# Optimization experiments

Measured on AMD Instinct MI355X. Metric: run time of the kernel, lower is better.

The kernel has to match this reference:

```python
import jax, jax.numpy as jnp
import numpy as np

B, T, D, H, S, PM = 2048, 128, 32, 256, 39, 12


def setup_inputs() -> dict:
    key = jax.random.key(0)
    ks = jax.random.split(key, 20)
    s = 0.05
    return {
        "x": jax.random.normal(ks[0], (B, T, D), jnp.float32),
        "latlons": jax.random.normal(ks[1], (B, 2), jnp.float32),
        "yearly_aggs": jax.random.normal(ks[2], (B, 37), jnp.float32),
        "pred_month": jax.random.uniform(ks[3], (B, PM), jnp.float32),
        # EA-LSTM cell parameters (Linear stores weight as [out,in])
        "Wf_i": jax.random.normal(ks[4], (H, D), jnp.float32) * s,
        "Wf_h": jax.random.normal(ks[5], (H, H), jnp.float32) * s,
        "bf_h": jnp.zeros((H,), jnp.float32),
        "Wu": jax.random.normal(ks[6], (H, S), jnp.float32) * s,
        "bu": jnp.zeros((H,), jnp.float32),
        "Wg_i": jax.random.normal(ks[7], (H, D), jnp.float32) * s,
        "Wg_h": jax.random.normal(ks[8], (H, H), jnp.float32) * s,
        "bg_h": jnp.zeros((H,), jnp.float32),
        "Wo_i": jax.random.normal(ks[9], (H, D), jnp.float32) * s,
        "Wo_h": jax.random.normal(ks[10], (H, H), jnp.float32) * s,
        "bo_h": jnp.zeros((H,), jnp.float32),
        # dense head: [268 -> 256 -> 1], no nonlinearity between layers (as in source)
        "Wd0": jax.random.normal(ks[11], (256, H + PM), jnp.float32) * s,
        "bd0": jnp.zeros((256,), jnp.float32),
        "Wd1": jax.random.normal(ks[12], (1, 256), jnp.float32) * s,
        "bd1": jnp.zeros((1,), jnp.float32),
    }


def reference(x, latlons, yearly_aggs, pred_month,
              Wf_i, Wf_h, bf_h, Wu, bu,
              Wg_i, Wg_h, bg_h, Wo_i, Wo_h, bo_h,
              Wd0, bd0, Wd1, bd1):
    x_s = jnp.concatenate([latlons, yearly_aggs], axis=-1)  # [B,S]
    i_gate = jax.nn.sigmoid(x_s @ Wu.T + bu)  # [B,H], static input gate

    # Precompute the input-to-gate projections for all timesteps (one big GEMM each)
    pf = jnp.einsum('btd,hd->tbh', x, Wf_i)  # [T,B,H]
    pg = jnp.einsum('btd,hd->tbh', x, Wg_i)
    po = jnp.einsum('btd,hd->tbh', x, Wo_i)

    h0 = jnp.zeros((x.shape[0], Wf_h.shape[0]), x.dtype)
    c0 = jnp.zeros_like(h0)

    def step(carry, inp):
        h, c = carry
        pf_t, pg_t, po_t = inp
        f = jax.nn.sigmoid(pf_t + h @ Wf_h.T + bf_h)
        g = jnp.tanh(pg_t + h @ Wg_h.T + bg_h)
        o = jax.nn.sigmoid(po_t + h @ Wo_h.T + bo_h)
        c1 = f * c + i_gate * g
        h1 = o * jnp.tanh(c1)
        return (h1, c1), None

    (h_last, _), _ = jax.lax.scan(step, (h0, c0), (pf, pg, po))

    # only the last hidden state feeds the dense head (dropout p=0 -> identity)
    z = jnp.concatenate([h_last, pred_month], axis=-1)  # [B, H+12]
    z = z @ Wd0.T + bd0
    z = z @ Wd1.T + bd1
    return z  # [B,1]
```

## Files before the change

kernel.cpp:

```cpp
#include <hip/hip_runtime.h>

typedef __bf16 bf16x8 __attribute__((ext_vector_type(8)));
typedef float  f32x4  __attribute__((ext_vector_type(4)));
typedef int    v4i    __attribute__((ext_vector_type(4)));

#define LOG2E 1.4426950408889634f

__device__ __forceinline__ float fexp(float x){ return __builtin_amdgcn_exp2f(x * LOG2E); }
__device__ __forceinline__ float sigm(float x){ return __builtin_amdgcn_rcpf(1.0f + fexp(-x)); }
__device__ __forceinline__ float ftanh(float x){
  float r = __builtin_amdgcn_rcpf(1.0f + __builtin_amdgcn_exp2f(-2.0f*LOG2E*x));
  return 2.0f*r - 1.0f;
}
__device__ __forceinline__ f32x4 MFMA(bf16x8 a, bf16x8 b, f32x4 c){
  return __builtin_amdgcn_mfma_f32_16x16x32_bf16(a, b, c, 0, 0, 0);
}
#define BC(w) __builtin_bit_cast(v4i, (w))

#define GRP_A(LEAD, A_, KT_) asm volatile(LEAD                  \
    "v_mfma_f32_16x16x32_bf16 %0, %6, %7, %0\n\t"               \
    "v_mfma_f32_16x16x32_bf16 %1, %6, %8, %1\n\t"               \
    "v_mfma_f32_16x16x32_bf16 %2, %6, %9, %2\n\t"               \
    "v_mfma_f32_16x16x32_bf16 %3, %6, %10, %3\n\t"              \
    "v_mfma_f32_16x16x32_bf16 %4, %6, %11, %4\n\t"              \
    "v_mfma_f32_16x16x32_bf16 %5, %6, %12, %5\n\t"              \
    "s_nop 3"                                                   \
    : "+v"(acc0),"+v"(acc1),"+v"(acc2),"+v"(acc3),"+v"(acc4),"+v"(acc5) \
    : "v"(A_), "a"(awf[(KT_)]),"a"(awf[(KT_)+5]),"a"(awf[(KT_)+10]),    \
      "a"(awf[(KT_)+15]),"a"(awf[(KT_)+20]),"a"(awf[(KT_)+25]))

#define GRP_V(A_, O_) asm volatile(                             \
    "v_mfma_f32_16x16x32_bf16 %0, %6, %7, %0\n\t"               \
    "v_mfma_f32_16x16x32_bf16 %1, %6, %8, %1\n\t"               \
    "v_mfma_f32_16x16x32_bf16 %2, %6, %9, %2\n\t"               \
    "v_mfma_f32_16x16x32_bf16 %3, %6, %10, %3\n\t"              \
    "v_mfma_f32_16x16x32_bf16 %4, %6, %11, %4\n\t"              \
    "v_mfma_f32_16x16x32_bf16 %5, %6, %12, %5\n\t"              \
    "s_nop 3"                                                   \
    : "+v"(acc0),"+v"(acc1),"+v"(acc2),"+v"(acc3),"+v"(acc4),"+v"(acc5) \
    : "v"(A_), "v"(wvf[(O_)]),"v"(wvf[(O_)+2]),"v"(wvf[(O_)+4]),        \
      "v"(wvf[(O_)+6]),"v"(wvf[(O_)+8]),"v"(wvf[(O_)+10]))

#define GRP_LX(A7_, AX_) asm volatile(                          \
    "ds_read_b128 %6, %14\n\t"                                  \
    "ds_read_b128 %7, %14 offset:1024\n\t"                      \
    "ds_read_b128 %8, %14 offset:16384\n\t"                     \
    "ds_read_b128 %9, %14 offset:17408\n\t"                     \
    "ds_read_b128 %10, %14 offset:32768\n\t"                    \
    "ds_read_b128 %11, %14 offset:33792\n\t"                    \
    "s_waitcnt lgkmcnt(0)\n\t"                                  \
    "v_mfma_f32_16x16x32_bf16 %0, %12, %6, %0\n\t"              \
    "v_mfma_f32_16x16x32_bf16 %1, %12, %7, %1\n\t"              \
    "v_mfma_f32_16x16x32_bf16 %2, %12, %8, %2\n\t"              \
    "v_mfma_f32_16x16x32_bf16 %3, %12, %9, %3\n\t"              \
    "v_mfma_f32_16x16x32_bf16 %4, %12, %10, %4\n\t"             \
    "v_mfma_f32_16x16x32_bf16 %5, %12, %11, %5\n\t"             \
    "ds_read_b128 %6, %15\n\t"                                  \
    "ds_read_b128 %7, %15 offset:1024\n\t"                      \
    "ds_read_b128 %8, %15 offset:16384\n\t"                     \
    "ds_read_b128 %9, %15 offset:17408\n\t"                     \
    "ds_read_b128 %10, %15 offset:32768\n\t"                    \
    "ds_read_b128 %11, %15 offset:33792\n\t"                    \
    "s_waitcnt lgkmcnt(0)\n\t"                                  \
    "v_mfma_f32_16x16x32_bf16 %0, %13, %6, %0\n\t"              \
    "v_mfma_f32_16x16x32_bf16 %1, %13, %7, %1\n\t"              \
    "v_mfma_f32_16x16x32_bf16 %2, %13, %8, %2\n\t"              \
    "v_mfma_f32_16x16x32_bf16 %3, %13, %9, %3\n\t"              \
    "v_mfma_f32_16x16x32_bf16 %4, %13, %10, %4\n\t"             \
    "v_mfma_f32_16x16x32_bf16 %5, %13, %11, %5\n\t"             \
    "s_nop 3"                                                   \
    : "+v"(acc0),"+v"(acc1),"+v"(acc2),"+v"(acc3),"+v"(acc4),"+v"(acc5), \
      "=&v"(t0),"=&v"(t1),"=&v"(t2),"=&v"(t3),"=&v"(t4),"=&v"(t5)        \
    : "v"(A7_), "v"(AX_), "v"(waddr0), "v"(waddr1))

#define BARRIER() asm volatile("s_waitcnt lgkmcnt(0)\n\ts_barrier" ::: "memory")

__global__ void
__attribute__((amdgpu_flat_work_group_size(512,512), amdgpu_waves_per_eu(2,2)))
ealstm_kernel(
    const float* __restrict__ x,      const float* __restrict__ latlons,
    const float* __restrict__ yearly, const float* __restrict__ pm,
    const float* __restrict__ Wf_i, const float* __restrict__ Wf_h, const float* __restrict__ bf_h,
    const float* __restrict__ Wu,   const float* __restrict__ bu,
    const float* __restrict__ Wg_i, const float* __restrict__ Wg_h, const float* __restrict__ bg_h,
    const float* __restrict__ Wo_i, const float* __restrict__ Wo_h, const float* __restrict__ bo_h,
    const float* __restrict__ Wd0,  const float* __restrict__ bd0,
    const float* __restrict__ Wd1,  const float* __restrict__ bd1,
    float* __restrict__ out)
{
  __shared__ __align__(16) __bf16 hbuf[2][4096];
  __shared__ __align__(16) __bf16 xbuf[2][16*40];
  __shared__ __align__(16) __bf16 wlds[2*48*512];
  __shared__ __align__(16) float  xs[16*64];

  const int tid  = threadIdx.x;
  const int w    = tid >> 6;
  const int lane = tid & 63;
  const int q    = lane >> 4;
  const int l    = lane & 15;
  const int wgb  = blockIdx.x * 8;

  const float* Wh[3] = {Wf_h, Wg_h, Wo_h};
  const float* Wi[3] = {Wf_i, Wg_i, Wo_i};

  for(int idx = tid; idx < 16*64; idx += 512){
    int m = idx >> 6, k = idx & 63;
    float v = 0.0f;
    if(m < 8){
      int b = wgb + m;
      if(k < 2) v = latlons[b*2 + k];
      else if(k < 39) v = yearly[b*37 + (k-2)];
    }
    xs[idx] = v;
  }
  for(int idx = tid; idx < 2*4096; idx += 512) ((__bf16*)hbuf)[idx] = (__bf16)0.0f;
  {
    int buf = tid >> 8, r = 8 + ((tid >> 5) & 7), c = tid & 31;
    xbuf[buf][r*40 + c] = (__bf16)0.0f;
  }
  if(tid < 256){
    int m = tid >> 5, k = tid & 31;
    xbuf[0][m*40 + k] = (__bf16)x[(size_t)(wgb + m)*4096 + k];
  }
  for(int grp = tid; grp < 2*48*64; grp += 512){
    int frag = grp >> 6, ln = grp & 63;
    int kk = frag / 48, f2 = frag % 48;
    int g = f2 >> 4, nt = f2 & 15;
    int q2 = ln >> 4, l2 = ln & 15;
    int cc = nt*16 + l2;
    const float* p = (kk == 0) ? (Wh[g] + cc*256 + 224 + q2*8)
                               : (Wi[g] + cc*32  + q2*8);
    bf16x8 v;
    #pragma unroll
    for(int j=0;j<8;j++) v[j] = (__bf16)p[j];
    *(bf16x8*)&wlds[frag*512 + ln*8] = v;
  }

  const int  srcl = lane & 31;
  const bool lo   = lane < 32;
  const int  qq4  = (q & 1) * 4;
  const int  colw = w*32 + ((lane & 32) >> 1) + l;
  const int  hwb  = (colw >> 5)*512 + qq4*32 + ((colw >> 3) & 3)*8 + (colw & 7);
  const unsigned waddr0 = (unsigned)(unsigned long long)&wlds[(0*48 + w*2)*512 + lane*8];
  const unsigned waddr1 = waddr0 + 49152u;
  const float b3f = bf_h[colw], b3g = bg_h[colw], b3o = bo_h[colw];

  __syncthreads();

  f32x4 igv;
  {
    float bu0 = bu[w*32 + l], bu1 = bu[w*32 + 16 + l];
    f32x4 iga0 = {bu0,bu0,bu0,bu0};
    f32x4 iga1 = {bu1,bu1,bu1,bu1};
    #pragma unroll
    for(int kt=0; kt<2; kt++){
      bf16x8 a;
      const float* xr = &xs[l*64 + kt*32 + q*8];
      #pragma unroll
      for(int j=0;j<8;j++) a[j] = (__bf16)xr[j];
      #pragma unroll
      for(int n=0;n<2;n++){
        int cc = w*32 + n*16 + l;
        bf16x8 b;
        #pragma unroll
        for(int j=0;j<8;j++){
          int k = kt*32 + q*8 + j;
          b[j] = (__bf16)((k < 39) ? Wu[cc*39 + k] : 0.0f);
        }
        if(n == 0) iga0 = MFMA(a, b, iga0); else iga1 = MFMA(a, b, iga1);
      }
    }
    #pragma unroll
    for(int i=0;i<4;i++){
      float s0 = sigm(iga0[i]);
      float s1 = __shfl(sigm(iga1[i]), srcl);
      igv[i] = lo ? s0 : s1;
    }
  }

  v4i wvf[12];
  #pragma unroll
  for(int f = 0; f < 12; f++){
    int gn = f >> 1, kt = 5 + (f & 1);
    int g = gn >> 1, n = gn & 1;
    int cc = w*32 + n*16 + l;
    const float* p = Wh[g] + cc*256 + kt*32 + q*8;
    f32x4 v0 = *(const f32x4*)p;
    f32x4 v1 = *(const f32x4*)(p + 4);
    bf16x8 v;
    v[0]=(__bf16)v0[0]; v[1]=(__bf16)v0[1]; v[2]=(__bf16)v0[2]; v[3]=(__bf16)v0[3];
    v[4]=(__bf16)v1[0]; v[5]=(__bf16)v1[1]; v[6]=(__bf16)v1[2]; v[7]=(__bf16)v1[3];
    wvf[f] = BC(v);
    if((f & 3) == 3) asm volatile("" ::: "memory");
  }
  v4i awf[30];
  #pragma unroll
  for(int f = 0; f < 30; f++){
    int gn = f / 5, kt = f % 5;
    int g = gn >> 1, n = gn & 1;
    int cc = w*32 + n*16 + l;
    const float* p = Wh[g] + cc*256 + kt*32 + q*8;
    f32x4 v0 = *(const f32x4*)p;
    f32x4 v1 = *(const f32x4*)(p + 4);
    bf16x8 v;
    v[0]=(__bf16)v0[0]; v[1]=(__bf16)v0[1]; v[2]=(__bf16)v0[2]; v[3]=(__bf16)v0[3];
    v[4]=(__bf16)v1[0]; v[5]=(__bf16)v1[1]; v[6]=(__bf16)v1[2]; v[7]=(__bf16)v1[3];
    asm("" : "=a"(awf[f]) : "0"(BC(v)));
    if((f % 5) == 4) asm volatile("" ::: "memory");
  }

  f32x4 cst = {0.f, 0.f, 0.f, 0.f};

  const int xri = (lane >> 2)*40 + (lane & 3)*8;
  const float* xbase = x + (size_t)(wgb + (lane >> 2))*4096 + (lane & 3)*8;
  f32x4 pv0 = {0.f,0.f,0.f,0.f}, pv1 = {0.f,0.f,0.f,0.f};
  if(w == 7 && lane < 32){
    pv0 = *(const f32x4*)(xbase + 32);
    pv1 = *(const f32x4*)(xbase + 36);
  }
  asm volatile("" ::: "memory");

#define LSTM_STEP(T_, CUR_)                                                     \
  {                                                                             \
      \
      \
    if(w == 7 && lane < 32){                                                    \
      if((T_) < 127){                                                           \
        bf16x8 v;                                                               \
        v[0]=(__bf16)pv0[0]; v[1]=(__bf16)pv0[1]; v[2]=(__bf16)pv0[2]; v[3]=(__bf16)pv0[3]; \
        v[4]=(__bf16)pv1[0]; v[5]=(__bf16)pv1[1]; v[6]=(__bf16)pv1[2]; v[7]=(__bf16)pv1[3]; \
        *(bf16x8*)&xbuf[(CUR_) ^ 1][xri] = v;                                   \
      }                                                                         \
      if((T_) < 126){                                                           \
        pv0 = *(const f32x4*)(xbase + ((T_)+2)*32);                             \
        pv1 = *(const f32x4*)(xbase + ((T_)+2)*32 + 4);                         \
      }                                                                         \
    }                                                                           \
    asm volatile("" ::: "memory");                                              \
    f32x4 z4 = {0.f,0.f,0.f,0.f};                                               \
    v4i acc0 = BC(z4), acc1 = BC(z4), acc2 = BC(z4);                            \
    v4i acc3 = BC(z4), acc4 = BC(z4), acc5 = BC(z4);                            \
    v4i t0, t1, t2, t3, t4, t5;                                                 \
    const __bf16* hb = hbuf[CUR_];                                              \
    { v4i a = BC(*(const bf16x8*)&hb[0*512 + l*32 + q*8]); GRP_A("s_nop 3\n\t", a, 0); } \
    { v4i a = BC(*(const bf16x8*)&hb[1*512 + l*32 + q*8]); GRP_A("", a, 1); }   \
    { v4i a = BC(*(const bf16x8*)&hb[2*512 + l*32 + q*8]); GRP_A("", a, 2); }   \
    { v4i a = BC(*(const bf16x8*)&hb[3*512 + l*32 + q*8]); GRP_A("", a, 3); }   \
    { v4i a = BC(*(const bf16x8*)&hb[4*512 + l*32 + q*8]); GRP_A("", a, 4); }   \
    { v4i a = BC(*(const bf16x8*)&hb[5*512 + l*32 + q*8]); GRP_V(a, 0); }       \
    { v4i a = BC(*(const bf16x8*)&hb[6*512 + l*32 + q*8]); GRP_V(a, 1); }       \
    { v4i a7 = BC(*(const bf16x8*)&hb[7*512 + l*32 + q*8]);                     \
      v4i ax = BC(*(const bf16x8*)&xbuf[CUR_][l*40 + q*8]);                     \
      GRP_LX(a7, ax); }                                                         \
    asm volatile("s_nop 7\n\ts_nop 7\n\ts_nop 7"                                \
      : "+v"(acc0),"+v"(acc1),"+v"(acc2),"+v"(acc3),"+v"(acc4),"+v"(acc5));     \
    f32x4 a0 = __builtin_bit_cast(f32x4, acc0);                                 \
    f32x4 a1 = __builtin_bit_cast(f32x4, acc1);                                 \
    f32x4 a2 = __builtin_bit_cast(f32x4, acc2);                                 \
    f32x4 a3 = __builtin_bit_cast(f32x4, acc3);                                 \
    f32x4 a4 = __builtin_bit_cast(f32x4, acc4);                                 \
    f32x4 a5 = __builtin_bit_cast(f32x4, acc5);                                 \
    _Pragma("unroll")                                                           \
    for(int i=0;i<4;i++){                                                       \
      float f1 = __shfl(a1[i], srcl);                                           \
      float g1 = __shfl(a3[i], srcl);                                           \
      float o1 = __shfl(a5[i], srcl);                                           \
      float fv = sigm ((lo ? a0[i] : f1) + b3f);                                \
      float gv = ftanh((lo ? a2[i] : g1) + b3g);                                \
      float ov = sigm ((lo ? a4[i] : o1) + b3o);                                \
      float cc = fv * cst[i] + igv[i] * gv;                                     \
      cst[i] = cc;                                                              \
      hbuf[(CUR_) ^ 1][hwb + i*32] = (__bf16)(ov * ftanh(cc));                  \
    }                                                                           \
    BARRIER();                                                                  \
  }

  #pragma unroll 1
  for(int tt = 0; tt < 64; tt++){
    LSTM_STEP(2*tt,     0)
    LSTM_STEP(2*tt + 1, 1)
  }
#undef LSTM_STEP

  f32x4 hd[2];
  { f32x4 z4 = {0.f,0.f,0.f,0.f}; hd[0] = z4; hd[1] = z4; }
  #pragma unroll 2
  for(int kt=0; kt<8; kt++){
    bf16x8 a = *(const bf16x8*)&hbuf[0][kt*512 + l*32 + q*8];
    #pragma unroll
    for(int n=0;n<2;n++){
      int cc = w*32 + n*16 + l;
      const float* p = Wd0 + cc*268 + kt*32 + q*8;
      bf16x8 b;
      #pragma unroll
      for(int j=0;j<8;j++) b[j] = (__bf16)p[j];
      hd[n] = MFMA(a, b, hd[n]);
    }
  }
  {
    bf16x8 a;
    #pragma unroll
    for(int j=0;j<8;j++){
      int k2 = q*8 + j;
      a[j] = (__bf16)((l < 8 && k2 < 12) ? pm[(size_t)(wgb + l)*12 + k2] : 0.0f);
    }
    #pragma unroll
    for(int n=0;n<2;n++){
      int cc = w*32 + n*16 + l;
      bf16x8 b;
      #pragma unroll
      for(int j=0;j<8;j++){
        int k2 = q*8 + j;
        b[j] = (__bf16)((k2 < 12) ? Wd0[cc*268 + 256 + k2] : 0.0f);
      }
      hd[n] = MFMA(a, b, hd[n]);
    }
  }
  float* z1 = (float*)wlds;
  #pragma unroll
  for(int n=0;n<2;n++){
    int cc = w*32 + n*16 + l;
    float bb = bd0[cc];
    #pragma unroll
    for(int i=0;i<4;i++) z1[(q*4 + i)*264 + cc] = hd[n][i] + bb;
  }
  __syncthreads();
  if(tid < 256){
    int row = tid >> 5, seg = tid & 31;
    const float* zr = &z1[row*264 + seg*8];
    const float* wr = Wd1 + seg*8;
    float s = 0.0f;
    #pragma unroll
    for(int j=0;j<8;j++) s += zr[j] * wr[j];
    s += __shfl_xor(s, 1);
    s += __shfl_xor(s, 2);
    s += __shfl_xor(s, 4);
    s += __shfl_xor(s, 8);
    s += __shfl_xor(s, 16);
    if(seg == 0) out[wgb + row] = s + bd1[0];
  }
}

extern "C" void kernel_launch(void* const* d_in, const int* in_sizes, int n_in,
                              void* d_out, int out_size, void* d_ws, size_t ws_size,
                              hipStream_t stream) {
  const float* x       = (const float*)d_in[0];
  const float* latlons = (const float*)d_in[1];
  const float* yearly  = (const float*)d_in[2];
  const float* pm      = (const float*)d_in[3];
  const float* Wf_i    = (const float*)d_in[4];
  const float* Wf_h    = (const float*)d_in[5];
  const float* bf_h    = (const float*)d_in[6];
  const float* Wu      = (const float*)d_in[7];
  const float* bu      = (const float*)d_in[8];
  const float* Wg_i    = (const float*)d_in[9];
  const float* Wg_h    = (const float*)d_in[10];
  const float* bg_h    = (const float*)d_in[11];
  const float* Wo_i    = (const float*)d_in[12];
  const float* Wo_h    = (const float*)d_in[13];
  const float* bo_h    = (const float*)d_in[14];
  const float* Wd0     = (const float*)d_in[15];
  const float* bd0     = (const float*)d_in[16];
  const float* Wd1     = (const float*)d_in[17];
  const float* bd1     = (const float*)d_in[18];

  ealstm_kernel<<<dim3(256), dim3(512), 0, stream>>>(
      x, latlons, yearly, pm,
      Wf_i, Wf_h, bf_h, Wu, bu,
      Wg_i, Wg_h, bg_h, Wo_i, Wo_h, bo_h,
      Wd0, bd0, Wd1, bd1,
      (float*)d_out);
}
```

Baseline: 354.9 us.

## Software-pipeline LSTM step tail: overlap gate activations with remaining MFMAs and LDS reads

Restructures the recurrent step tail so the forget, cell and output gate accumulators are finished in separate stages. Each stage's nonlinearity (exp/rcp) and cross-half permlane32 swap runs while the next gate's MFMAs and the next LDS weight prefetches are in flight. Weight fragments for the first K tile are prefetched across the barrier into the next step. Two weight fragments move to AGPRs, and the x staging is split across two waves with 4-wide writes. The aim is to hide activation latency and LDS wait behind matrix work on the serial critical path. The cost is heavy hand-written asm with manual hazard nops and tighter register pressure.

```diff
diff --git a/kernel.cpp b/kernel.cpp
--- a/kernel.cpp
+++ b/kernel.cpp
@@ -1,6 +1,7 @@
 #include <hip/hip_runtime.h>
 
 typedef __bf16 bf16x8 __attribute__((ext_vector_type(8)));
+typedef __bf16 bf16x4 __attribute__((ext_vector_type(4)));
 typedef float  f32x4  __attribute__((ext_vector_type(4)));
 typedef int    v4i    __attribute__((ext_vector_type(4)));
 
@@ -41,37 +42,17 @@
     : "v"(A_), "v"(wvf[(O_)]),"v"(wvf[(O_)+2]),"v"(wvf[(O_)+4]),        \
       "v"(wvf[(O_)+6]),"v"(wvf[(O_)+8]),"v"(wvf[(O_)+10]))
 
-#define GRP_LX(A7_, AX_) asm volatile(                          \
-    "ds_read_b128 %6, %14\n\t"                                  \
-    "ds_read_b128 %7, %14 offset:1024\n\t"                      \
-    "ds_read_b128 %8, %14 offset:16384\n\t"                     \
-    "ds_read_b128 %9, %14 offset:17408\n\t"                     \
-    "ds_read_b128 %10, %14 offset:32768\n\t"                    \
-    "ds_read_b128 %11, %14 offset:33792\n\t"                    \
-    "s_waitcnt lgkmcnt(0)\n\t"                                  \
-    "v_mfma_f32_16x16x32_bf16 %0, %12, %6, %0\n\t"              \
-    "v_mfma_f32_16x16x32_bf16 %1, %12, %7, %1\n\t"              \
-    "v_mfma_f32_16x16x32_bf16 %2, %12, %8, %2\n\t"              \
-    "v_mfma_f32_16x16x32_bf16 %3, %12, %9, %3\n\t"              \
-    "v_mfma_f32_16x16x32_bf16 %4, %12, %10, %4\n\t"             \
-    "v_mfma_f32_16x16x32_bf16 %5, %12, %11, %5\n\t"             \
-    "ds_read_b128 %6, %15\n\t"                                  \
-    "ds_read_b128 %7, %15 offset:1024\n\t"                      \
-    "ds_read_b128 %8, %15 offset:16384\n\t"                     \
-    "ds_read_b128 %9, %15 offset:17408\n\t"                     \
-    "ds_read_b128 %10, %15 offset:32768\n\t"                    \
-    "ds_read_b128 %11, %15 offset:33792\n\t"                    \
-    "s_waitcnt lgkmcnt(0)\n\t"                                  \
-    "v_mfma_f32_16x16x32_bf16 %0, %13, %6, %0\n\t"              \
-    "v_mfma_f32_16x16x32_bf16 %1, %13, %7, %1\n\t"              \
-    "v_mfma_f32_16x16x32_bf16 %2, %13, %8, %2\n\t"              \
-    "v_mfma_f32_16x16x32_bf16 %3, %13, %9, %3\n\t"              \
-    "v_mfma_f32_16x16x32_bf16 %4, %13, %10, %4\n\t"             \
-    "v_mfma_f32_16x16x32_bf16 %5, %13, %11, %5\n\t"             \
+#define GRP_V6(A_) asm volatile(                                \
+    "v_mfma_f32_16x16x32_bf16 %0, %6, %7, %0\n\t"               \
+    "v_mfma_f32_16x16x32_bf16 %1, %6, %8, %1\n\t"               \
+    "v_mfma_f32_16x16x32_bf16 %2, %6, %9, %2\n\t"               \
+    "v_mfma_f32_16x16x32_bf16 %3, %6, %10, %3\n\t"              \
+    "v_mfma_f32_16x16x32_bf16 %4, %6, %11, %4\n\t"              \
+    "v_mfma_f32_16x16x32_bf16 %5, %6, %12, %5\n\t"              \
     "s_nop 3"                                                   \
-    : "+v"(acc0),"+v"(acc1),"+v"(acc2),"+v"(acc3),"+v"(acc4),"+v"(acc5), \
-      "=&v"(t0),"=&v"(t1),"=&v"(t2),"=&v"(t3),"=&v"(t4),"=&v"(t5)        \
-    : "v"(A7_), "v"(AX_), "v"(waddr0), "v"(waddr1))
+    : "+v"(acc0),"+v"(acc1),"+v"(acc2),"+v"(acc3),"+v"(acc4),"+v"(acc5) \
+    : "v"(A_), "v"(wvf[1]),"v"(wvf[3]),"v"(wvf[5]),"v"(wvf[7]),         \
+      "a"(aw6o0),"a"(aw6o1))
 
 #define BARRIER() asm volatile("s_waitcnt lgkmcnt(0)\n\ts_barrier" ::: "memory")
 
@@ -143,6 +124,8 @@
   const int  hwb  = (colw >> 5)*512 + qq4*32 + ((colw >> 3) & 3)*8 + (colw & 7);
   const unsigned waddr0 = (unsigned)(unsigned long long)&wlds[(0*48 + w*2)*512 + lane*8];
   const unsigned waddr1 = waddr0 + 49152u;
+  const unsigned hA0 = (unsigned)(unsigned long long)&hbuf[0][l*32 + q*8];
+  const unsigned xA0 = (unsigned)(unsigned long long)&xbuf[0][l*40 + q*8];
   const float b3f = bf_h[colw], b3g = bg_h[colw], b3o = bo_h[colw];
 
   __syncthreads();
@@ -179,6 +162,7 @@
   }
 
   v4i wvf[12];
+  v4i aw6o0, aw6o1;
   #pragma unroll
   for(int f = 0; f < 12; f++){
     int gn = f >> 1, kt = 5 + (f & 1);
@@ -190,7 +174,9 @@
     bf16x8 v;
     v[0]=(__bf16)v0[0]; v[1]=(__bf16)v0[1]; v[2]=(__bf16)v0[2]; v[3]=(__bf16)v0[3];
     v[4]=(__bf16)v1[0]; v[5]=(__bf16)v1[1]; v[6]=(__bf16)v1[2]; v[7]=(__bf16)v1[3];
-    wvf[f] = BC(v);
+    if(f == 9)       asm("" : "=a"(aw6o0) : "0"(BC(v)));
+    else if(f == 11) asm("" : "=a"(aw6o1) : "0"(BC(v)));
+    else             wvf[f] = BC(v);
     if((f & 3) == 3) asm volatile("" ::: "memory");
   }
   v4i awf[30];
@@ -211,36 +197,47 @@
 
   f32x4 cst = {0.f, 0.f, 0.f, 0.f};
 
-  const int xri = (lane >> 2)*40 + (lane & 3)*8;
-  const float* xbase = x + (size_t)(wgb + (lane >> 2))*4096 + (lane & 3)*8;
-  f32x4 pv0 = {0.f,0.f,0.f,0.f}, pv1 = {0.f,0.f,0.f,0.f};
-  if(w == 7 && lane < 32){
-    pv0 = *(const f32x4*)(xbase + 32);
-    pv1 = *(const f32x4*)(xbase + 36);
-  }
+  const int wio = (w == 7) ? 4 : 0;
+  const int xri = (lane >> 2)*40 + (lane & 3)*8 + wio;
+  const float* xbase = x + (size_t)(wgb + (lane >> 2))*4096 + (lane & 3)*8 + wio;
+  f32x4 pv = {0.f,0.f,0.f,0.f};
+  if(w >= 6 && lane < 32) pv = *(const f32x4*)(xbase + 32);
   asm volatile("" ::: "memory");
+
+  v4i t0, t1, t2, t3, t4, t5;
+  asm volatile(
+    "ds_read_b128 %0, %6\n\t"
+    "ds_read_b128 %1, %6 offset:1024\n\t"
+    "ds_read_b128 %2, %7\n\t"
+    "ds_read_b128 %3, %7 offset:1024\n\t"
+    "ds_read_b128 %4, %6 offset:16384\n\t"
+    "ds_read_b128 %5, %6 offset:17408"
+    : "=v"(t0),"=v"(t1),"=v"(t2),"=v"(t3),"=v"(t4),"=v"(t5)
+    : "v"(waddr0),"v"(waddr1));
 
 #define LSTM_STEP(T_, CUR_)                                                     \
   {                                                                             \
-      \
-      \
-    if(w == 7 && lane < 32){                                                    \
+    if(w >= 6 && lane < 32){                                                    \
       if((T_) < 127){                                                           \
-        bf16x8 v;                                                               \
-        v[0]=(__bf16)pv0[0]; v[1]=(__bf16)pv0[1]; v[2]=(__bf16)pv0[2]; v[3]=(__bf16)pv0[3]; \
-        v[4]=(__bf16)pv1[0]; v[5]=(__bf16)pv1[1]; v[6]=(__bf16)pv1[2]; v[7]=(__bf16)pv1[3]; \
-        *(bf16x8*)&xbuf[(CUR_) ^ 1][xri] = v;                                   \
+        bf16x4 v4;                                                              \
+        v4[0]=(__bf16)pv[0]; v4[1]=(__bf16)pv[1];                               \
+        v4[2]=(__bf16)pv[2]; v4[3]=(__bf16)pv[3];                               \
+        *(bf16x4*)&xbuf[(CUR_) ^ 1][xri] = v4;                                  \
       }                                                                         \
-      if((T_) < 126){                                                           \
-        pv0 = *(const f32x4*)(xbase + ((T_)+2)*32);                             \
-        pv1 = *(const f32x4*)(xbase + ((T_)+2)*32 + 4);                         \
-      }                                                                         \
+      if((T_) < 126) pv = *(const f32x4*)(xbase + ((T_)+2)*32);                 \
     }                                                                           \
     asm volatile("" ::: "memory");                                              \
+    v4i A7, Axv;                                                                \
+    {                                                                           \
+      unsigned hAc = hA0 + (CUR_)*8192u;                                        \
+      unsigned xAc = xA0 + (CUR_)*1280u;                                        \
+      asm volatile("ds_read_b128 %0, %2 offset:7168\n\t"                        \
+                   "ds_read_b128 %1, %3"                                        \
+                   : "=v"(A7), "=v"(Axv) : "v"(hAc), "v"(xAc));                 \
+    }                                                                           \
     f32x4 z4 = {0.f,0.f,0.f,0.f};                                               \
     v4i acc0 = BC(z4), acc1 = BC(z4), acc2 = BC(z4);                            \
     v4i acc3 = BC(z4), acc4 = BC(z4), acc5 = BC(z4);                            \
-    v4i t0, t1, t2, t3, t4, t5;                                                 \
     const __bf16* hb = hbuf[CUR_];                                              \
     { v4i a = BC(*(const bf16x8*)&hb[0*512 + l*32 + q*8]); GRP_A("s_nop 3\n\t", a, 0); } \
     { v4i a = BC(*(const bf16x8*)&hb[1*512 + l*32 + q*8]); GRP_A("", a, 1); }   \
@@ -248,30 +245,148 @@
     { v4i a = BC(*(const bf16x8*)&hb[3*512 + l*32 + q*8]); GRP_A("", a, 3); }   \
     { v4i a = BC(*(const bf16x8*)&hb[4*512 + l*32 + q*8]); GRP_A("", a, 4); }   \
     { v4i a = BC(*(const bf16x8*)&hb[5*512 + l*32 + q*8]); GRP_V(a, 0); }       \
-    { v4i a = BC(*(const bf16x8*)&hb[6*512 + l*32 + q*8]); GRP_V(a, 1); }       \
-    { v4i a7 = BC(*(const bf16x8*)&hb[7*512 + l*32 + q*8]);                     \
-      v4i ax = BC(*(const bf16x8*)&xbuf[CUR_][l*40 + q*8]);                     \
-      GRP_LX(a7, ax); }                                                         \
-    asm volatile("s_nop 7\n\ts_nop 7\n\ts_nop 7"                                \
-      : "+v"(acc0),"+v"(acc1),"+v"(acc2),"+v"(acc3),"+v"(acc4),"+v"(acc5));     \
-    f32x4 a0 = __builtin_bit_cast(f32x4, acc0);                                 \
-    f32x4 a1 = __builtin_bit_cast(f32x4, acc1);                                 \
-    f32x4 a2 = __builtin_bit_cast(f32x4, acc2);                                 \
-    f32x4 a3 = __builtin_bit_cast(f32x4, acc3);                                 \
-    f32x4 a4 = __builtin_bit_cast(f32x4, acc4);                                 \
-    f32x4 a5 = __builtin_bit_cast(f32x4, acc5);                                 \
-    _Pragma("unroll")                                                           \
-    for(int i=0;i<4;i++){                                                       \
-      float f1 = __shfl(a1[i], srcl);                                           \
-      float g1 = __shfl(a3[i], srcl);                                           \
-      float o1 = __shfl(a5[i], srcl);                                           \
-      float fv = sigm ((lo ? a0[i] : f1) + b3f);                                \
-      float gv = ftanh((lo ? a2[i] : g1) + b3g);                                \
-      float ov = sigm ((lo ? a4[i] : o1) + b3o);                                \
-      float cc = fv * cst[i] + igv[i] * gv;                                     \
-      cst[i] = cc;                                                              \
-      hbuf[(CUR_) ^ 1][hwb + i*32] = (__bf16)(ov * ftanh(cc));                  \
-    }                                                                           \
+    { v4i a = BC(*(const bf16x8*)&hb[6*512 + l*32 + q*8]); GRP_V6(a); }         \
+      \
+      \
+      \
+    asm volatile(                                                               \
+      "s_waitcnt lgkmcnt(0)\n\t"                                                \
+      "v_mfma_f32_16x16x32_bf16 %0, %6, %2, %0\n\t"                             \
+      "v_mfma_f32_16x16x32_bf16 %1, %6, %3, %1\n\t"                             \
+      "s_nop 2\n\t"                                                             \
+      "v_mfma_f32_16x16x32_bf16 %0, %7, %4, %0\n\t"                             \
+      "v_mfma_f32_16x16x32_bf16 %1, %7, %5, %1\n\t"                             \
+      "ds_read_b128 %2, %9 offset:16384\n\t"                                    \
+      "ds_read_b128 %3, %9 offset:17408\n\t"                                    \
+      "ds_read_b128 %4, %8 offset:32768\n\t"                                    \
+      "ds_read_b128 %5, %8 offset:33792\n\t"                                    \
+      "s_nop 7\n\t"                                                             \
+      "s_nop 7\n\t"                                                             \
+      "s_nop 7\n\t"                                                             \
+      "s_nop 7"                                                                 \
+      : "+v"(acc0),"+v"(acc1),"+v"(t0),"+v"(t1),"+v"(t2),"+v"(t3)               \
+      : "v"(A7),"v"(Axv),"v"(waddr0),"v"(waddr1));                              \
+    f32x4 vf0 = __builtin_bit_cast(f32x4, acc0);                                \
+    f32x4 vf1 = __builtin_bit_cast(f32x4, acc1);                                \
+    float fa0=vf0[0], fa1=vf0[1], fa2=vf0[2], fa3=vf0[3];                       \
+    float fb0=vf1[0], fb1=vf1[1], fb2=vf1[2], fb3=vf1[3];                       \
+     \
+    asm volatile(                                                               \
+      "v_mfma_f32_16x16x32_bf16 %0, %14, %10, %0\n\t"                           \
+      "v_mfma_f32_16x16x32_bf16 %1, %14, %11, %1\n\t"                           \
+      "s_nop 2\n\t"                                                             \
+      "v_permlane32_swap_b32 %2, %6\n\t"                                        \
+      "v_permlane32_swap_b32 %3, %7\n\t"                                        \
+      "v_permlane32_swap_b32 %4, %8\n\t"                                        \
+      "v_permlane32_swap_b32 %5, %9\n\t"                                        \
+      "v_add_f32 %2, %2, %16\n\t"                                               \
+      "v_add_f32 %3, %3, %16\n\t"                                               \
+      "v_add_f32 %4, %4, %16\n\t"                                               \
+      "v_add_f32 %5, %5, %16\n\t"                                               \
+      "v_mul_f32 %2, 0xbfb8aa3b, %2\n\t"                                        \
+      "v_mul_f32 %3, 0xbfb8aa3b, %3\n\t"                                        \
+      "v_mul_f32 %4, 0xbfb8aa3b, %4\n\t"                                        \
+      "v_mul_f32 %5, 0xbfb8aa3b, %5\n\t"                                        \
+      "v_exp_f32 %2, %2\n\t"                                                    \
+      "v_exp_f32 %3, %3\n\t"                                                    \
+      "v_exp_f32 %4, %4\n\t"                                                    \
+      "v_exp_f32 %5, %5\n\t"                                                    \
+      "v_add_f32 %2, 1.0, %2\n\t"                                               \
+      "v_add_f32 %3, 1.0, %3\n\t"                                               \
+      "v_add_f32 %4, 1.0, %4\n\t"                                               \
+      "v_add_f32 %5, 1.0, %5\n\t"                                               \
+      "v_rcp_f32 %2, %2\n\t"                                                    \
+      "v_rcp_f32 %3, %3\n\t"                                                    \
+      "v_rcp_f32 %4, %4\n\t"                                                    \
+      "v_rcp_f32 %5, %5\n\t"                                                    \
+      "s_waitcnt lgkmcnt(2)\n\t"                                                \
+      "v_mfma_f32_16x16x32_bf16 %0, %15, %12, %0\n\t"                           \
+      "v_mfma_f32_16x16x32_bf16 %1, %15, %13, %1\n\t"                           \
+      "ds_read_b128 %10, %17 offset:32768\n\t"                                  \
+      "ds_read_b128 %11, %17 offset:33792\n\t"                                  \
+      "s_nop 7\n\t"                                                             \
+      "s_nop 7\n\t"                                                             \
+      "s_nop 7\n\t"                                                             \
+      "s_nop 7"                                                                 \
+      : "+v"(acc2),"+v"(acc3),"+v"(fa0),"+v"(fa1),"+v"(fa2),"+v"(fa3),          \
+        "+v"(fb0),"+v"(fb1),"+v"(fb2),"+v"(fb3),"+v"(t4),"+v"(t5)               \
+      : "v"(t0),"v"(t1),"v"(A7),"v"(Axv),"v"(b3f),"v"(waddr1));                 \
+    f32x4 vg0 = __builtin_bit_cast(f32x4, acc2);                                \
+    f32x4 vg1 = __builtin_bit_cast(f32x4, acc3);                                \
+    float ga0=vg0[0], ga1=vg0[1], ga2=vg0[2], ga3=vg0[3];                       \
+    float gb0=vg1[0], gb1=vg1[1], gb2=vg1[2], gb3=vg1[3];                       \
+     \
+    asm volatile(                                                               \
+      "s_waitcnt lgkmcnt(2)\n\t"                                                \
+      "v_mfma_f32_16x16x32_bf16 %0, %16, %12, %0\n\t"                           \
+      "v_mfma_f32_16x16x32_bf16 %1, %16, %13, %1\n\t"                           \
+      "s_nop 2\n\t"                                                             \
+      "v_permlane32_swap_b32 %2, %6\n\t"                                        \
+      "v_permlane32_swap_b32 %3, %7\n\t"                                        \
+      "v_permlane32_swap_b32 %4, %8\n\t"                                        \
+      "v_permlane32_swap_b32 %5, %9\n\t"                                        \
+      "v_add_f32 %2, %2, %18\n\t"                                               \
+      "v_add_f32 %3, %3, %18\n\t"                                               \
+      "v_add_f32 %4, %4, %18\n\t"                                               \
+      "v_add_f32 %5, %5, %18\n\t"                                               \
+      "v_mul_f32 %2, 0xc038aa3b, %2\n\t"                                        \
+      "v_mul_f32 %3, 0xc038aa3b, %3\n\t"                                        \
+      "v_mul_f32 %4, 0xc038aa3b, %4\n\t"                                        \
+      "v_mul_f32 %5, 0xc038aa3b, %5\n\t"                                        \
+      "v_exp_f32 %2, %2\n\t"                                                    \
+      "v_exp_f32 %3, %3\n\t"                                                    \
+      "v_exp_f32 %4, %4\n\t"                                                    \
+      "v_exp_f32 %5, %5\n\t"                                                    \
+      "v_add_f32 %2, 1.0, %2\n\t"                                               \
+      "v_add_f32 %3, 1.0, %3\n\t"                                               \
+      "v_add_f32 %4, 1.0, %4\n\t"                                               \
+      "v_add_f32 %5, 1.0, %5\n\t"                                               \
+      "v_rcp_f32 %2, %2\n\t"                                                    \
+      "v_rcp_f32 %3, %3\n\t"                                                    \
+      "v_rcp_f32 %4, %4\n\t"                                                    \
+      "v_rcp_f32 %5, %5\n\t"                                                    \
+      "v_fma_f32 %2, %2, 2.0, -1.0\n\t"                                         \
+      "v_fma_f32 %3, %3, 2.0, -1.0\n\t"                                         \
+      "v_fma_f32 %4, %4, 2.0, -1.0\n\t"                                         \
+      "v_fma_f32 %5, %5, 2.0, -1.0\n\t"                                         \
+      "s_waitcnt lgkmcnt(0)\n\t"                                                \
+      "v_mfma_f32_16x16x32_bf16 %0, %17, %14, %0\n\t"                           \
+      "v_mfma_f32_16x16x32_bf16 %1, %17, %15, %1\n\t"                           \
+      "ds_read_b128 %10, %19\n\t"                                               \
+      "ds_read_b128 %11, %19 offset:1024\n\t"                                   \
+      "ds_read_b128 %12, %20\n\t"                                               \
+      "ds_read_b128 %13, %20 offset:1024\n\t"                                   \
+      "ds_read_b128 %14, %19 offset:16384\n\t"                                  \
+      "ds_read_b128 %15, %19 offset:17408\n\t"                                  \
+      "s_nop 7\n\t"                                                             \
+      "s_nop 7\n\t"                                                             \
+      "s_nop 7\n\t"                                                             \
+      "s_nop 7"                                                                 \
+      : "+v"(acc4),"+v"(acc5),"+v"(ga0),"+v"(ga1),"+v"(ga2),"+v"(ga3),          \
+        "+v"(gb0),"+v"(gb1),"+v"(gb2),"+v"(gb3),                                \
+        "+v"(t0),"+v"(t1),"+v"(t2),"+v"(t3),"+v"(t4),"+v"(t5)                   \
+      : "v"(A7),"v"(Axv),"v"(b3g),"v"(waddr0),"v"(waddr1));                     \
+    f32x4 vo0 = __builtin_bit_cast(f32x4, acc4);                                \
+    f32x4 vo1 = __builtin_bit_cast(f32x4, acc5);                                \
+    float oa0=vo0[0], oa1=vo0[1], oa2=vo0[2], oa3=vo0[3];                       \
+    float ob0=vo1[0], ob1=vo1[1], ob2=vo1[2], ob3=vo1[3];                       \
+    asm volatile(                                                               \
+      "s_nop 1\n\t"                                                             \
+      "v_permlane32_swap_b32 %0, %4\n\t"                                        \
+      "v_permlane32_swap_b32 %1, %5\n\t"                                        \
+      "v_permlane32_swap_b32 %2, %6\n\t"                                        \
+      "v_permlane32_swap_b32 %3, %7"                                            \
+      : "+v"(oa0),"+v"(oa1),"+v"(oa2),"+v"(oa3),                                \
+        "+v"(ob0),"+v"(ob1),"+v"(ob2),"+v"(ob3));                               \
+    __bf16* hbw = &hbuf[(CUR_) ^ 1][hwb];                                       \
+    { float ov = sigm(oa0 + b3o); float cc = fa0*cst[0] + igv[0]*ga0;           \
+      cst[0] = cc; hbw[0]  = (__bf16)(ov * ftanh(cc)); }                        \
+    { float ov = sigm(oa1 + b3o); float cc = fa1*cst[1] + igv[1]*ga1;           \
+      cst[1] = cc; hbw[32] = (__bf16)(ov * ftanh(cc)); }                        \
+    { float ov = sigm(oa2 + b3o); float cc = fa2*cst[2] + igv[2]*ga2;           \
+      cst[2] = cc; hbw[64] = (__bf16)(ov * ftanh(cc)); }                        \
+    { float ov = sigm(oa3 + b3o); float cc = fa3*cst[3] + igv[3]*ga3;           \
+      cst[3] = cc; hbw[96] = (__bf16)(ov * ftanh(cc)); }                        \
     BARRIER();                                                                  \
   }
 
```

Result: slower. 398.5 us (+12.3%).

## Split recurrent columns across 16 waves with all weights held in AGPRs

Applied to the files above, without the earlier changes.

Doubles the workgroup to 1024 threads (16 waves), so each wave owns 16 hidden columns instead of 32. That lets all recurrent and input weights for a wave sit in accumulation registers, which removes the LDS weight staging, the per-step LDS weight reads and the cross-lane shuffles that stitched two column tiles together. Each step now issues fewer MFMAs per wave, with more waves per CU contending at the barrier. The extra registers and the larger barrier group may cost occupancy or add sync overhead.

```diff
diff --git a/kernel.cpp b/kernel.cpp
--- a/kernel.cpp
+++ b/kernel.cpp
@@ -17,66 +17,26 @@
 }
 #define BC(w) __builtin_bit_cast(v4i, (w))
 
-#define GRP_A(LEAD, A_, KT_) asm volatile(LEAD                  \
-    "v_mfma_f32_16x16x32_bf16 %0, %6, %7, %0\n\t"               \
-    "v_mfma_f32_16x16x32_bf16 %1, %6, %8, %1\n\t"               \
-    "v_mfma_f32_16x16x32_bf16 %2, %6, %9, %2\n\t"               \
-    "v_mfma_f32_16x16x32_bf16 %3, %6, %10, %3\n\t"              \
-    "v_mfma_f32_16x16x32_bf16 %4, %6, %11, %4\n\t"              \
-    "v_mfma_f32_16x16x32_bf16 %5, %6, %12, %5\n\t"              \
+#define GRP3(LEAD, A_, KT_) asm volatile(LEAD                   \
+    "v_mfma_f32_16x16x32_bf16 %0, %3, %4, %0\n\t"               \
+    "v_mfma_f32_16x16x32_bf16 %1, %3, %5, %1\n\t"               \
+    "v_mfma_f32_16x16x32_bf16 %2, %3, %6, %2\n\t"               \
     "s_nop 3"                                                   \
-    : "+v"(acc0),"+v"(acc1),"+v"(acc2),"+v"(acc3),"+v"(acc4),"+v"(acc5) \
-    : "v"(A_), "a"(awf[(KT_)]),"a"(awf[(KT_)+5]),"a"(awf[(KT_)+10]),    \
-      "a"(awf[(KT_)+15]),"a"(awf[(KT_)+20]),"a"(awf[(KT_)+25]))
-
-#define GRP_V(A_, O_) asm volatile(                             \
-    "v_mfma_f32_16x16x32_bf16 %0, %6, %7, %0\n\t"               \
-    "v_mfma_f32_16x16x32_bf16 %1, %6, %8, %1\n\t"               \
-    "v_mfma_f32_16x16x32_bf16 %2, %6, %9, %2\n\t"               \
-    "v_mfma_f32_16x16x32_bf16 %3, %6, %10, %3\n\t"              \
-    "v_mfma_f32_16x16x32_bf16 %4, %6, %11, %4\n\t"              \
-    "v_mfma_f32_16x16x32_bf16 %5, %6, %12, %5\n\t"              \
+    : "+v"(accf),"+v"(accg),"+v"(acco)                          \
+    : "v"(A_), "a"(awh[(KT_)]), "a"(awh[(KT_)+8]), "a"(awh[(KT_)+16]))
+
+#define GRPX(A_) asm volatile(                                  \
+    "v_mfma_f32_16x16x32_bf16 %0, %3, %4, %0\n\t"               \
+    "v_mfma_f32_16x16x32_bf16 %1, %3, %5, %1\n\t"               \
+    "v_mfma_f32_16x16x32_bf16 %2, %3, %6, %2\n\t"               \
     "s_nop 3"                                                   \
-    : "+v"(acc0),"+v"(acc1),"+v"(acc2),"+v"(acc3),"+v"(acc4),"+v"(acc5) \
-    : "v"(A_), "v"(wvf[(O_)]),"v"(wvf[(O_)+2]),"v"(wvf[(O_)+4]),        \
-      "v"(wvf[(O_)+6]),"v"(wvf[(O_)+8]),"v"(wvf[(O_)+10]))
-
-#define GRP_LX(A7_, AX_) asm volatile(                          \
-    "ds_read_b128 %6, %14\n\t"                                  \
-    "ds_read_b128 %7, %14 offset:1024\n\t"                      \
-    "ds_read_b128 %8, %14 offset:16384\n\t"                     \
-    "ds_read_b128 %9, %14 offset:17408\n\t"                     \
-    "ds_read_b128 %10, %14 offset:32768\n\t"                    \
-    "ds_read_b128 %11, %14 offset:33792\n\t"                    \
-    "s_waitcnt lgkmcnt(0)\n\t"                                  \
-    "v_mfma_f32_16x16x32_bf16 %0, %12, %6, %0\n\t"              \
-    "v_mfma_f32_16x16x32_bf16 %1, %12, %7, %1\n\t"              \
-    "v_mfma_f32_16x16x32_bf16 %2, %12, %8, %2\n\t"              \
-    "v_mfma_f32_16x16x32_bf16 %3, %12, %9, %3\n\t"              \
-    "v_mfma_f32_16x16x32_bf16 %4, %12, %10, %4\n\t"             \
-    "v_mfma_f32_16x16x32_bf16 %5, %12, %11, %5\n\t"             \
-    "ds_read_b128 %6, %15\n\t"                                  \
-    "ds_read_b128 %7, %15 offset:1024\n\t"                      \
-    "ds_read_b128 %8, %15 offset:16384\n\t"                     \
-    "ds_read_b128 %9, %15 offset:17408\n\t"                     \
-    "ds_read_b128 %10, %15 offset:32768\n\t"                    \
-    "ds_read_b128 %11, %15 offset:33792\n\t"                    \
-    "s_waitcnt lgkmcnt(0)\n\t"                                  \
-    "v_mfma_f32_16x16x32_bf16 %0, %13, %6, %0\n\t"              \
-    "v_mfma_f32_16x16x32_bf16 %1, %13, %7, %1\n\t"              \
-    "v_mfma_f32_16x16x32_bf16 %2, %13, %8, %2\n\t"              \
-    "v_mfma_f32_16x16x32_bf16 %3, %13, %9, %3\n\t"              \
-    "v_mfma_f32_16x16x32_bf16 %4, %13, %10, %4\n\t"             \
-    "v_mfma_f32_16x16x32_bf16 %5, %13, %11, %5\n\t"             \
-    "s_nop 3"                                                   \
-    : "+v"(acc0),"+v"(acc1),"+v"(acc2),"+v"(acc3),"+v"(acc4),"+v"(acc5), \
-      "=&v"(t0),"=&v"(t1),"=&v"(t2),"=&v"(t3),"=&v"(t4),"=&v"(t5)        \
-    : "v"(A7_), "v"(AX_), "v"(waddr0), "v"(waddr1))
+    : "+v"(accf),"+v"(accg),"+v"(acco)                          \
+    : "v"(A_), "a"(awx[0]), "a"(awx[1]), "a"(awx[2]))
 
 #define BARRIER() asm volatile("s_waitcnt lgkmcnt(0)\n\ts_barrier" ::: "memory")
 
 __global__ void
-__attribute__((amdgpu_flat_work_group_size(512,512), amdgpu_waves_per_eu(2,2)))
+__attribute__((amdgpu_flat_work_group_size(1024,1024), amdgpu_waves_per_eu(4,4)))
 ealstm_kernel(
     const float* __restrict__ x,      const float* __restrict__ latlons,
     const float* __restrict__ yearly, const float* __restrict__ pm,
@@ -90,8 +50,8 @@
 {
   __shared__ __align__(16) __bf16 hbuf[2][4096];
   __shared__ __align__(16) __bf16 xbuf[2][16*40];
-  __shared__ __align__(16) __bf16 wlds[2*48*512];
   __shared__ __align__(16) float  xs[16*64];
+  __shared__ __align__(16) float  z1s[8*264];
 
   const int tid  = threadIdx.x;
   const int w    = tid >> 6;
@@ -99,22 +59,22 @@
   const int q    = lane >> 4;
   const int l    = lane & 15;
   const int wgb  = blockIdx.x * 8;
+  const int colc = w*16 + l;
 
   const float* Wh[3] = {Wf_h, Wg_h, Wo_h};
   const float* Wi[3] = {Wf_i, Wg_i, Wo_i};
 
-  for(int idx = tid; idx < 16*64; idx += 512){
-    int m = idx >> 6, k = idx & 63;
+  { int m = tid >> 6, k = tid & 63;
     float v = 0.0f;
     if(m < 8){
       int b = wgb + m;
       if(k < 2) v = latlons[b*2 + k];
       else if(k < 39) v = yearly[b*37 + (k-2)];
     }
-    xs[idx] = v;
-  }
-  for(int idx = tid; idx < 2*4096; idx += 512) ((__bf16*)hbuf)[idx] = (__bf16)0.0f;
-  {
+    xs[tid] = v;
+  }
+  for(int idx = tid; idx < 2*4096; idx += 1024) ((__bf16*)hbuf)[idx] = (__bf16)0.0f;
+  if(tid < 512){
     int buf = tid >> 8, r = 8 + ((tid >> 5) & 7), c = tid & 31;
     xbuf[buf][r*40 + c] = (__bf16)0.0f;
   }
@@ -122,99 +82,67 @@
     int m = tid >> 5, k = tid & 31;
     xbuf[0][m*40 + k] = (__bf16)x[(size_t)(wgb + m)*4096 + k];
   }
-  for(int grp = tid; grp < 2*48*64; grp += 512){
-    int frag = grp >> 6, ln = grp & 63;
-    int kk = frag / 48, f2 = frag % 48;
-    int g = f2 >> 4, nt = f2 & 15;
-    int q2 = ln >> 4, l2 = ln & 15;
-    int cc = nt*16 + l2;
-    const float* p = (kk == 0) ? (Wh[g] + cc*256 + 224 + q2*8)
-                               : (Wi[g] + cc*32  + q2*8);
-    bf16x8 v;
-    #pragma unroll
-    for(int j=0;j<8;j++) v[j] = (__bf16)p[j];
-    *(bf16x8*)&wlds[frag*512 + ln*8] = v;
-  }
-
-  const int  srcl = lane & 31;
-  const bool lo   = lane < 32;
-  const int  qq4  = (q & 1) * 4;
-  const int  colw = w*32 + ((lane & 32) >> 1) + l;
-  const int  hwb  = (colw >> 5)*512 + qq4*32 + ((colw >> 3) & 3)*8 + (colw & 7);
-  const unsigned waddr0 = (unsigned)(unsigned long long)&wlds[(0*48 + w*2)*512 + lane*8];
-  const unsigned waddr1 = waddr0 + 49152u;
-  const float b3f = bf_h[colw], b3g = bg_h[colw], b3o = bo_h[colw];
+
+  const int  hwb = (colc >> 5)*512 + q*128 + (colc & 31);
+  const bool stl = (lane < 32);
+  const float b3f = bf_h[colc], b3g = bg_h[colc], b3o = bo_h[colc];
 
   __syncthreads();
 
   f32x4 igv;
   {
-    float bu0 = bu[w*32 + l], bu1 = bu[w*32 + 16 + l];
-    f32x4 iga0 = {bu0,bu0,bu0,bu0};
-    f32x4 iga1 = {bu1,bu1,bu1,bu1};
+    float bu0 = bu[colc];
+    f32x4 iga = {bu0,bu0,bu0,bu0};
     #pragma unroll
     for(int kt=0; kt<2; kt++){
       bf16x8 a;
       const float* xr = &xs[l*64 + kt*32 + q*8];
       #pragma unroll
       for(int j=0;j<8;j++) a[j] = (__bf16)xr[j];
+      bf16x8 b;
       #pragma unroll
-      for(int n=0;n<2;n++){
-        int cc = w*32 + n*16 + l;
-        bf16x8 b;
-        #pragma unroll
-        for(int j=0;j<8;j++){
-          int k = kt*32 + q*8 + j;
-          b[j] = (__bf16)((k < 39) ? Wu[cc*39 + k] : 0.0f);
-        }
-        if(n == 0) iga0 = MFMA(a, b, iga0); else iga1 = MFMA(a, b, iga1);
+      for(int j=0;j<8;j++){
+        int k = kt*32 + q*8 + j;
+        b[j] = (__bf16)((k < 39) ? Wu[colc*39 + k] : 0.0f);
       }
-    }
-    #pragma unroll
-    for(int i=0;i<4;i++){
-      float s0 = sigm(iga0[i]);
-      float s1 = __shfl(sigm(iga1[i]), srcl);
-      igv[i] = lo ? s0 : s1;
-    }
-  }
-
-  v4i wvf[12];
+      iga = MFMA(a, b, iga);
+    }
+    #pragma unroll
+    for(int i=0;i<4;i++) igv[i] = sigm(iga[i]);
+  }
+
+  v4i awh[24];
   #pragma unroll
-  for(int f = 0; f < 12; f++){
-    int gn = f >> 1, kt = 5 + (f & 1);
-    int g = gn >> 1, n = gn & 1;
-    int cc = w*32 + n*16 + l;
-    const float* p = Wh[g] + cc*256 + kt*32 + q*8;
+  for(int f = 0; f < 24; f++){
+    int g = f >> 3, kt = f & 7;
+    const float* p = Wh[g] + colc*256 + kt*32 + q*8;
     f32x4 v0 = *(const f32x4*)p;
     f32x4 v1 = *(const f32x4*)(p + 4);
     bf16x8 v;
     v[0]=(__bf16)v0[0]; v[1]=(__bf16)v0[1]; v[2]=(__bf16)v0[2]; v[3]=(__bf16)v0[3];
     v[4]=(__bf16)v1[0]; v[5]=(__bf16)v1[1]; v[6]=(__bf16)v1[2]; v[7]=(__bf16)v1[3];
-    wvf[f] = BC(v);
+    asm("" : "=a"(awh[f]) : "0"(BC(v)));
     if((f & 3) == 3) asm volatile("" ::: "memory");
   }
-  v4i awf[30];
+  v4i awx[3];
   #pragma unroll
-  for(int f = 0; f < 30; f++){
-    int gn = f / 5, kt = f % 5;
-    int g = gn >> 1, n = gn & 1;
-    int cc = w*32 + n*16 + l;
-    const float* p = Wh[g] + cc*256 + kt*32 + q*8;
+  for(int g = 0; g < 3; g++){
+    const float* p = Wi[g] + colc*32 + q*8;
     f32x4 v0 = *(const f32x4*)p;
     f32x4 v1 = *(const f32x4*)(p + 4);
     bf16x8 v;
     v[0]=(__bf16)v0[0]; v[1]=(__bf16)v0[1]; v[2]=(__bf16)v0[2]; v[3]=(__bf16)v0[3];
     v[4]=(__bf16)v1[0]; v[5]=(__bf16)v1[1]; v[6]=(__bf16)v1[2]; v[7]=(__bf16)v1[3];
-    asm("" : "=a"(awf[f]) : "0"(BC(v)));
-    if((f % 5) == 4) asm volatile("" ::: "memory");
-  }
+    asm("" : "=a"(awx[g]) : "0"(BC(v)));
+  }
+  asm volatile("" ::: "memory");
 
   f32x4 cst = {0.f, 0.f, 0.f, 0.f};
 
   const int xri = (lane >> 2)*40 + (lane & 3)*8;
   const float* xbase = x + (size_t)(wgb + (lane >> 2))*4096 + (lane & 3)*8;
   f32x4 pv0 = {0.f,0.f,0.f,0.f}, pv1 = {0.f,0.f,0.f,0.f};
-  if(w == 7 && lane < 32){
+  if(w == 15 && lane < 32){
     pv0 = *(const f32x4*)(xbase + 32);
     pv1 = *(const f32x4*)(xbase + 36);
   }
@@ -222,9 +150,7 @@
 
 #define LSTM_STEP(T_, CUR_)                                                     \
   {                                                                             \
-      \
-      \
-    if(w == 7 && lane < 32){                                                    \
+    if(w == 15 && lane < 32){                                                   \
       if((T_) < 127){                                                           \
         bf16x8 v;                                                               \
         v[0]=(__bf16)pv0[0]; v[1]=(__bf16)pv0[1]; v[2]=(__bf16)pv0[2]; v[3]=(__bf16)pv0[3]; \
@@ -238,39 +164,38 @@
     }                                                                           \
     asm volatile("" ::: "memory");                                              \
     f32x4 z4 = {0.f,0.f,0.f,0.f};                                               \
-    v4i acc0 = BC(z4), acc1 = BC(z4), acc2 = BC(z4);                            \
-    v4i acc3 = BC(z4), acc4 = BC(z4), acc5 = BC(z4);                            \
-    v4i t0, t1, t2, t3, t4, t5;                                                 \
+    v4i accf = BC(z4), accg = BC(z4), acco = BC(z4);                            \
     const __bf16* hb = hbuf[CUR_];                                              \
-    { v4i a = BC(*(const bf16x8*)&hb[0*512 + l*32 + q*8]); GRP_A("s_nop 3\n\t", a, 0); } \
-    { v4i a = BC(*(const bf16x8*)&hb[1*512 + l*32 + q*8]); GRP_A("", a, 1); }   \
-    { v4i a = BC(*(const bf16x8*)&hb[2*512 + l*32 + q*8]); GRP_A("", a, 2); }   \
-    { v4i a = BC(*(const bf16x8*)&hb[3*512 + l*32 + q*8]); GRP_A("", a, 3); }   \
-    { v4i a = BC(*(const bf16x8*)&hb[4*512 + l*32 + q*8]); GRP_A("", a, 4); }   \
-    { v4i a = BC(*(const bf16x8*)&hb[5*512 + l*32 + q*8]); GRP_V(a, 0); }       \
-    { v4i a = BC(*(const bf16x8*)&hb[6*512 + l*32 + q*8]); GRP_V(a, 1); }       \
-    { v4i a7 = BC(*(const bf16x8*)&hb[7*512 + l*32 + q*8]);                     \
-      v4i ax = BC(*(const bf16x8*)&xbuf[CUR_][l*40 + q*8]);                     \
-      GRP_LX(a7, ax); }                                                         \
-    asm volatile("s_nop 7\n\ts_nop 7\n\ts_nop 7"                                \
-      : "+v"(acc0),"+v"(acc1),"+v"(acc2),"+v"(acc3),"+v"(acc4),"+v"(acc5));     \
-    f32x4 a0 = __builtin_bit_cast(f32x4, acc0);                                 \
-    f32x4 a1 = __builtin_bit_cast(f32x4, acc1);                                 \
-    f32x4 a2 = __builtin_bit_cast(f32x4, acc2);                                 \
-    f32x4 a3 = __builtin_bit_cast(f32x4, acc3);                                 \
-    f32x4 a4 = __builtin_bit_cast(f32x4, acc4);                                 \
-    f32x4 a5 = __builtin_bit_cast(f32x4, acc5);                                 \
-    _Pragma("unroll")                                                           \
-    for(int i=0;i<4;i++){                                                       \
-      float f1 = __shfl(a1[i], srcl);                                           \
-      float g1 = __shfl(a3[i], srcl);                                           \
-      float o1 = __shfl(a5[i], srcl);                                           \
-      float fv = sigm ((lo ? a0[i] : f1) + b3f);                                \
-      float gv = ftanh((lo ? a2[i] : g1) + b3g);                                \
-      float ov = sigm ((lo ? a4[i] : o1) + b3o);                                \
-      float cc = fv * cst[i] + igv[i] * gv;                                     \
-      cst[i] = cc;                                                              \
-      hbuf[(CUR_) ^ 1][hwb + i*32] = (__bf16)(ov * ftanh(cc));                  \
+    { v4i a = BC(*(const bf16x8*)&hb[0*512 + l*32 + q*8]); GRP3("s_nop 3\n\t", a, 0); } \
+    { v4i a = BC(*(const bf16x8*)&hb[1*512 + l*32 + q*8]); GRP3("", a, 1); }    \
+    { v4i a = BC(*(const bf16x8*)&hb[2*512 + l*32 + q*8]); GRP3("", a, 2); }    \
+    { v4i a = BC(*(const bf16x8*)&hb[3*512 + l*32 + q*8]); GRP3("", a, 3); }    \
+    { v4i a = BC(*(const bf16x8*)&hb[4*512 + l*32 + q*8]); GRP3("", a, 4); }    \
+    { v4i a = BC(*(const bf16x8*)&hb[5*512 + l*32 + q*8]); GRP3("", a, 5); }    \
+    { v4i a = BC(*(const bf16x8*)&hb[6*512 + l*32 + q*8]); GRP3("", a, 6); }    \
+    { v4i a = BC(*(const bf16x8*)&hb[7*512 + l*32 + q*8]); GRP3("", a, 7); }    \
+    { v4i a = BC(*(const bf16x8*)&xbuf[CUR_][l*40 + q*8]); GRPX(a); }           \
+               \
+    asm volatile("s_nop 7\n\ts_nop 7\n\ts_nop 7\n\ts_nop 3"                     \
+      : "+v"(accf),"+v"(accg),"+v"(acco));                                      \
+    f32x4 af = __builtin_bit_cast(f32x4, accf);                                 \
+    f32x4 ag = __builtin_bit_cast(f32x4, accg);                                 \
+    f32x4 ao = __builtin_bit_cast(f32x4, acco);                                 \
+    float h0, h1, h2, h3;                                                       \
+    { float fv=sigm(af[0]+b3f), gv=ftanh(ag[0]+b3g), ov=sigm(ao[0]+b3o);        \
+      float cc=fv*cst[0]+igv[0]*gv; cst[0]=cc; h0 = ov*ftanh(cc); }             \
+    { float fv=sigm(af[1]+b3f), gv=ftanh(ag[1]+b3g), ov=sigm(ao[1]+b3o);        \
+      float cc=fv*cst[1]+igv[1]*gv; cst[1]=cc; h1 = ov*ftanh(cc); }             \
+    { float fv=sigm(af[2]+b3f), gv=ftanh(ag[2]+b3g), ov=sigm(ao[2]+b3o);        \
+      float cc=fv*cst[2]+igv[2]*gv; cst[2]=cc; h2 = ov*ftanh(cc); }             \
+    { float fv=sigm(af[3]+b3f), gv=ftanh(ag[3]+b3g), ov=sigm(ao[3]+b3o);        \
+      float cc=fv*cst[3]+igv[3]*gv; cst[3]=cc; h3 = ov*ftanh(cc); }             \
+    if(stl){                                                                    \
+      __bf16* hbw = &hbuf[(CUR_) ^ 1][hwb];                                     \
+      hbw[0]  = (__bf16)h0;                                                     \
+      hbw[32] = (__bf16)h1;                                                     \
+      hbw[64] = (__bf16)h2;                                                     \
+      hbw[96] = (__bf16)h3;                                                     \
     }                                                                           \
     BARRIER();                                                                  \
   }
@@ -282,52 +207,37 @@
   }
 #undef LSTM_STEP
 
-  f32x4 hd[2];
-  { f32x4 z4 = {0.f,0.f,0.f,0.f}; hd[0] = z4; hd[1] = z4; }
+  f32x4 hd = {0.f,0.f,0.f,0.f};
   #pragma unroll 2
   for(int kt=0; kt<8; kt++){
     bf16x8 a = *(const bf16x8*)&hbuf[0][kt*512 + l*32 + q*8];
-    #pragma unroll
-    for(int n=0;n<2;n++){
-      int cc = w*32 + n*16 + l;
-      const float* p = Wd0 + cc*268 + kt*32 + q*8;
-      bf16x8 b;
-      #pragma unroll
-      for(int j=0;j<8;j++) b[j] = (__bf16)p[j];
-      hd[n] = MFMA(a, b, hd[n]);
-    }
+    bf16x8 b;
+    const float* p = Wd0 + colc*268 + kt*32 + q*8;
+    #pragma unroll
+    for(int j=0;j<8;j++) b[j] = (__bf16)p[j];
+    hd = MFMA(a, b, hd);
   }
   {
-    bf16x8 a;
+    bf16x8 a, b;
     #pragma unroll
     for(int j=0;j<8;j++){
       int k2 = q*8 + j;
       a[j] = (__bf16)((l < 8 && k2 < 12) ? pm[(size_t)(wgb + l)*12 + k2] : 0.0f);
-    }
-    #pragma unroll
-    for(int n=0;n<2;n++){
-      int cc = w*32 + n*16 + l;
-      bf16x8 b;
+      b[j] = (__bf16)((k2 < 12) ? Wd0[colc*268 + 256 + k2] : 0.0f);
+    }
+    hd = MFMA(a, b, hd);
+  }
+  {
+    float bb = bd0[colc];
+    if(stl){
       #pragma unroll
-      for(int j=0;j<8;j++){
-        int k2 = q*8 + j;
-        b[j] = (__bf16)((k2 < 12) ? Wd0[cc*268 + 256 + k2] : 0.0f);
-      }
-      hd[n] = MFMA(a, b, hd[n]);
-    }
-  }
-  float* z1 = (float*)wlds;
-  #pragma unroll
-  for(int n=0;n<2;n++){
-    int cc = w*32 + n*16 + l;
-    float bb = bd0[cc];
-    #pragma unroll
-    for(int i=0;i<4;i++) z1[(q*4 + i)*264 + cc] = hd[n][i] + bb;
+      for(int i=0;i<4;i++) z1s[(q*4 + i)*264 + colc] = hd[i] + bb;
+    }
   }
   __syncthreads();
   if(tid < 256){
     int row = tid >> 5, seg = tid & 31;
-    const float* zr = &z1[row*264 + seg*8];
+    const float* zr = &z1s[row*264 + seg*8];
     const float* wr = Wd1 + seg*8;
     float s = 0.0f;
     #pragma unroll
@@ -364,7 +274,7 @@
   const float* Wd1     = (const float*)d_in[17];
   const float* bd1     = (const float*)d_in[18];
 
-  ealstm_kernel<<<dim3(256), dim3(512), 0, stream>>>(
+  ealstm_kernel<<<dim3(256), dim3(1024), 0, stream>>>(
       x, latlons, yearly, pm,
       Wf_i, Wf_h, bf_h, Wu, bu,
       Wg_i, Wg_h, bg_h, Wo_i, Wo_h, bo_h,
```

After: 747.7 us. 2.11x slower.
